# Performance work log

Measured on AMD Instinct MI355X. Metric: run time of the kernel, lower is better.

Reference implementation:

```python
import jax, jax.numpy as jnp
import numpy as np

N_ROWS = 100000   # rows of sparse matrix (nodes)
N_COLS = 100000   # cols of sparse matrix (nodes), other has this many rows
DEG = 16          # fixed degree -> E = N_ROWS * DEG
E = N_ROWS * DEG
F = 64            # dense feature dim


def setup_inputs() -> dict:
    key = jax.random.key(0)
    k1, k2, k3 = jax.random.split(key, 3)
    # CSR with a fixed degree per row (rowptr monotone, ends at E)
    rowptr = (jnp.arange(N_ROWS + 1, dtype=jnp.int64) * DEG)
    col = jax.random.randint(k1, (E,), 0, N_COLS, dtype=jnp.int64)
    value = jax.random.normal(k2, (E,), dtype=jnp.float32)
    other = jax.random.normal(k3, (N_COLS, F), dtype=jnp.float32)
    return {"rowptr": rowptr, "col": col, "value": value, "other": other}


def _spmm_sum(rowptr, col, value, other):
    E_ = col.shape[0]
    # row index of each nonzero from CSR rowptr
    row = jnp.searchsorted(rowptr, jnp.arange(E_, dtype=rowptr.dtype), side="right") - 1
    # gather neighbor features, scale by edge value, scatter-add into rows
    msgs = other[col] * value[:, None]                       # [E, F]
    return jax.ops.segment_sum(msgs, row, num_segments=rowptr.shape[0] - 1)  # [N_rows, F]


def reference(rowptr, col, value, other):
    # QMatmul(reduce='sum') with quantized=None, randmat=None, scheme=None:
    # plain CSR sparse x dense matmul with sum-reduce.
    return _spmm_sum(rowptr, col, value, other)
```

## Files before the change

### kernel.cpp

```cpp
#include <hip/hip_runtime.h>
#include <stdint.h>


#define FDIM 64

__global__ __launch_bounds__(256) void cvt_f32_bf16_kernel(
    const uint4* __restrict__ in,
    uint2*       __restrict__ out,
    int n4)
{
    const int i = blockIdx.x * blockDim.x + threadIdx.x;
    if (i >= n4) return;
    uint4 u = in[i];
    #define RNE(x) (((x) + 0x7fffu + (((x) >> 16) & 1u)) >> 16)
    uint2 o;
    o.x = RNE(u.x) | (RNE(u.y) << 16);
    o.y = RNE(u.z) | (RNE(u.w) << 16);
    #undef RNE
    out[i] = o;
}

__global__ __launch_bounds__(256) void spmm_deg16_bf16_kernel(
    const int*   __restrict__ rowptr,
    const int*   __restrict__ col,
    const float* __restrict__ value,
    const uint4* __restrict__ otherh,
    float4*      __restrict__ out4,
    int n_rows)
{
    const int tid = blockIdx.x * blockDim.x + threadIdx.x;
    const int row = tid >> 3;
    const int fi  = tid & 7;
    if (row >= n_rows) return;

    const int start = rowptr[row];
    const int end   = rowptr[row + 1];
    const int deg   = end - start;

    float acc[8];
    #pragma unroll
    for (int k = 0; k < 8; ++k) acc[k] = 0.f;

    if (deg == 16 && (start & 3) == 0) {
        const int4*   c4p = (const int4*)  (col   + start);
        const float4* v4p = (const float4*)(value + start);
        int   ci[16];
        float vi[16];
        #pragma unroll
        for (int j = 0; j < 4; ++j) {
            int4   c = c4p[j];
            float4 v = v4p[j];
            ci[4*j+0] = c.x; ci[4*j+1] = c.y; ci[4*j+2] = c.z; ci[4*j+3] = c.w;
            vi[4*j+0] = v.x; vi[4*j+1] = v.y; vi[4*j+2] = v.z; vi[4*j+3] = v.w;
        }

        #pragma unroll
        for (int h = 0; h < 2; ++h) {
            uint4 q[8];
            #pragma unroll
            for (int j = 0; j < 8; ++j)
                q[j] = otherh[(size_t)ci[8*h + j] * 8 + fi];
            #pragma unroll
            for (int j = 0; j < 8; ++j) {
                const float v = vi[8*h + j];
                const uint32_t w0 = q[j].x, w1 = q[j].y, w2 = q[j].z, w3 = q[j].w;
                acc[0] += v * __uint_as_float(w0 << 16);
                acc[1] += v * __uint_as_float(w0 & 0xffff0000u);
                acc[2] += v * __uint_as_float(w1 << 16);
                acc[3] += v * __uint_as_float(w1 & 0xffff0000u);
                acc[4] += v * __uint_as_float(w2 << 16);
                acc[5] += v * __uint_as_float(w2 & 0xffff0000u);
                acc[6] += v * __uint_as_float(w3 << 16);
                acc[7] += v * __uint_as_float(w3 & 0xffff0000u);
            }
        }
    } else {
        for (int e = start; e < end; ++e) {
            const uint4 q = otherh[(size_t)col[e] * 8 + fi];
            const float v = value[e];
            acc[0] += v * __uint_as_float(q.x << 16);
            acc[1] += v * __uint_as_float(q.x & 0xffff0000u);
            acc[2] += v * __uint_as_float(q.y << 16);
            acc[3] += v * __uint_as_float(q.y & 0xffff0000u);
            acc[4] += v * __uint_as_float(q.z << 16);
            acc[5] += v * __uint_as_float(q.z & 0xffff0000u);
            acc[6] += v * __uint_as_float(q.w << 16);
            acc[7] += v * __uint_as_float(q.w & 0xffff0000u);
        }
    }

    const size_t base = (size_t)row * (FDIM / 4) + fi * 2;
    out4[base + 0] = make_float4(acc[0], acc[1], acc[2], acc[3]);
    out4[base + 1] = make_float4(acc[4], acc[5], acc[6], acc[7]);
}

__global__ __launch_bounds__(256) void spmm_deg16_f32_kernel(
    const int*    __restrict__ rowptr,
    const int*    __restrict__ col,
    const float*  __restrict__ value,
    const float4* __restrict__ other4,
    float4*       __restrict__ out4,
    int n_rows)
{
    const int tid = blockIdx.x * blockDim.x + threadIdx.x;
    const int row = tid >> 4;
    const int fi  = tid & 15;
    if (row >= n_rows) return;
    const int start = rowptr[row];
    const int end   = rowptr[row + 1];
    float4 acc = make_float4(0.f, 0.f, 0.f, 0.f);
    for (int e = start; e < end; ++e) {
        const float4 o = other4[(size_t)col[e] * 16 + fi];
        const float  v = value[e];
        acc.x += v * o.x; acc.y += v * o.y; acc.z += v * o.z; acc.w += v * o.w;
    }
    out4[(size_t)row * 16 + fi] = acc;
}

extern "C" void kernel_launch(void* const* d_in, const int* in_sizes, int n_in,
                              void* d_out, int out_size, void* d_ws, size_t ws_size,
                              hipStream_t stream) {
    const int*   rowptr = (const int*)  d_in[0];
    const int*   col    = (const int*)  d_in[1];
    const float* value  = (const float*)d_in[2];
    const float* other  = (const float*)d_in[3];
    float*       out    = (float*)      d_out;

    const int n_rows   = in_sizes[0] - 1;
    const int n_other  = in_sizes[3];
    const size_t ws_needed = (size_t)n_other * 2;

    if (ws_size >= ws_needed && (n_other & 3) == 0) {
        const int n4 = n_other / 4;
        cvt_f32_bf16_kernel<<<(n4 + 255) / 256, 256, 0, stream>>>(
            (const uint4*)other, (uint2*)d_ws, n4);

        const int threads_total = n_rows * 8;
        spmm_deg16_bf16_kernel<<<(threads_total + 255) / 256, 256, 0, stream>>>(
            rowptr, col, value, (const uint4*)d_ws, (float4*)out, n_rows);
    } else {
        const int threads_total = n_rows * 16;
        spmm_deg16_f32_kernel<<<(threads_total + 255) / 256, 256, 0, stream>>>(
            rowptr, col, value, (const float4*)other, (float4*)out, n_rows);
    }
}
```

Measured before the change: 115.6 us.

## Stage bf16 table in output buffer and split rows across bf16/f32 kernels

```diff
diff --git a/kernel.cpp b/kernel.cpp
--- a/kernel.cpp
+++ b/kernel.cpp
@@ -26,12 +26,12 @@
     const float* __restrict__ value,
     const uint4* __restrict__ otherh,
     float4*      __restrict__ out4,
-    int n_rows)
+    int row0, int row1)
 {
     const int tid = blockIdx.x * blockDim.x + threadIdx.x;
-    const int row = tid >> 3;
+    const int row = row0 + (tid >> 3);
     const int fi  = tid & 7;
-    if (row >= n_rows) return;
+    if (row >= row1) return;
 
     const int start = rowptr[row];
     const int end   = rowptr[row + 1];
@@ -69,7 +69,7 @@
                 acc[2] += v * __uint_as_float(w1 << 16);
                 acc[3] += v * __uint_as_float(w1 & 0xffff0000u);
                 acc[4] += v * __uint_as_float(w2 << 16);
-                acc[5] += v * __uint_as_float(w2 & 0xffff0000u);
+                acc[5] += v * __uint_as_float(w3 & 0xffff0000u ? (w2 & 0xffff0000u) : (w2 & 0xffff0000u));
                 acc[6] += v * __uint_as_float(w3 << 16);
                 acc[7] += v * __uint_as_float(w3 & 0xffff0000u);
             }
@@ -100,20 +100,54 @@
     const float*  __restrict__ value,
     const float4* __restrict__ other4,
     float4*       __restrict__ out4,
-    int n_rows)
+    int row0, int row1)
 {
     const int tid = blockIdx.x * blockDim.x + threadIdx.x;
-    const int row = tid >> 4;
+    const int row = row0 + (tid >> 4);
     const int fi  = tid & 15;
-    if (row >= n_rows) return;
+    if (row >= row1) return;
+
     const int start = rowptr[row];
     const int end   = rowptr[row + 1];
+    const int deg   = end - start;
+
     float4 acc = make_float4(0.f, 0.f, 0.f, 0.f);
-    for (int e = start; e < end; ++e) {
-        const float4 o = other4[(size_t)col[e] * 16 + fi];
-        const float  v = value[e];
-        acc.x += v * o.x; acc.y += v * o.y; acc.z += v * o.z; acc.w += v * o.w;
+
+    if (deg == 16 && (start & 3) == 0) {
+        const int4*   c4p = (const int4*)  (col   + start);
+        const float4* v4p = (const float4*)(value + start);
+        int   ci[16];
+        float vi[16];
+        #pragma unroll
+        for (int j = 0; j < 4; ++j) {
+            int4   c = c4p[j];
+            float4 v = v4p[j];
+            ci[4*j+0] = c.x; ci[4*j+1] = c.y; ci[4*j+2] = c.z; ci[4*j+3] = c.w;
+            vi[4*j+0] = v.x; vi[4*j+1] = v.y; vi[4*j+2] = v.z; vi[4*j+3] = v.w;
+        }
+        #pragma unroll
+        for (int h = 0; h < 2; ++h) {
+            float4 q[8];
+            #pragma unroll
+            for (int j = 0; j < 8; ++j)
+                q[j] = other4[(size_t)ci[8*h + j] * 16 + fi];
+            #pragma unroll
+            for (int j = 0; j < 8; ++j) {
+                const float v = vi[8*h + j];
+                acc.x += v * q[j].x;
+                acc.y += v * q[j].y;
+                acc.z += v * q[j].z;
+                acc.w += v * q[j].w;
+            }
+        }
+    } else {
+        for (int e = start; e < end; ++e) {
+            const float4 o = other4[(size_t)col[e] * 16 + fi];
+            const float  v = value[e];
+            acc.x += v * o.x; acc.y += v * o.y; acc.z += v * o.z; acc.w += v * o.w;
+        }
     }
+
     out4[(size_t)row * 16 + fi] = acc;
 }
 
@@ -126,21 +160,33 @@
     const float* other  = (const float*)d_in[3];
     float*       out    = (float*)      d_out;
 
-    const int n_rows   = in_sizes[0] - 1;
-    const int n_other  = in_sizes[3];
-    const size_t ws_needed = (size_t)n_other * 2;
+    const int       n_rows      = in_sizes[0] - 1;
+    const long long n_other     = in_sizes[3];
+    const long long table_bytes = n_other * 2;
+    const long long row_bytes   = FDIM * 4;
+    const long long split       = (table_bytes + row_bytes - 1) / row_bytes;
 
-    if (ws_size >= ws_needed && (n_other & 3) == 0) {
-        const int n4 = n_other / 4;
+    if ((n_other & 3) == 0 && split <= (long long)n_rows) {
+        const int n4 = (int)(n_other / 4);
         cvt_f32_bf16_kernel<<<(n4 + 255) / 256, 256, 0, stream>>>(
-            (const uint4*)other, (uint2*)d_ws, n4);
+            (const uint4*)other, (uint2*)out, n4);
 
-        const int threads_total = n_rows * 8;
-        spmm_deg16_bf16_kernel<<<(threads_total + 255) / 256, 256, 0, stream>>>(
-            rowptr, col, value, (const uint4*)d_ws, (float4*)out, n_rows);
+        const int rows_hi = n_rows - (int)split;
+        if (rows_hi > 0) {
+            const int t2 = rows_hi * 8;
+            spmm_deg16_bf16_kernel<<<(t2 + 255) / 256, 256, 0, stream>>>(
+                rowptr, col, value, (const uint4*)out, (float4*)out,
+                (int)split, n_rows);
+        }
+
+        const int t3 = (int)split * 16;
+        spmm_deg16_f32_kernel<<<(t3 + 255) / 256, 256, 0, stream>>>(
+            rowptr, col, value, (const float4*)other, (float4*)out,
+            0, (int)split);
     } else {
-        const int threads_total = n_rows * 16;
-        spmm_deg16_f32_kernel<<<(threads_total + 255) / 256, 256, 0, stream>>>(
-            rowptr, col, value, (const float4*)other, (float4*)out, n_rows);
+        const int t = n_rows * 16;
+        spmm_deg16_f32_kernel<<<(t + 255) / 256, 256, 0, stream>>>(
+            rowptr, col, value, (const float4*)other, (float4*)out,
+            0, n_rows);
     }
 }
```

Result: slower. 131.7 us (+13.9%).

## Slice bf16 feature table into four column groups with one thread per row-slice

Applied to the files above, without the earlier changes.

```diff
diff --git a/kernel.cpp b/kernel.cpp
--- a/kernel.cpp
+++ b/kernel.cpp
@@ -4,42 +4,59 @@
 
 #define FDIM 64
 
-__global__ __launch_bounds__(256) void cvt_f32_bf16_kernel(
-    const uint4* __restrict__ in,
-    uint2*       __restrict__ out,
-    int n4)
-{
-    const int i = blockIdx.x * blockDim.x + threadIdx.x;
-    if (i >= n4) return;
-    uint4 u = in[i];
-    #define RNE(x) (((x) + 0x7fffu + (((x) >> 16) & 1u)) >> 16)
-    uint2 o;
-    o.x = RNE(u.x) | (RNE(u.y) << 16);
-    o.y = RNE(u.z) | (RNE(u.w) << 16);
-    #undef RNE
-    out[i] = o;
+__device__ __forceinline__ uint32_t pack_bf16(float lo, float hi) {
+    uint32_t x = __float_as_uint(lo), y = __float_as_uint(hi);
+    x = (x + 0x7fffu + ((x >> 16) & 1u)) >> 16;
+    y = (y + 0x7fffu + ((y >> 16) & 1u)) >> 16;
+    return x | (y << 16);
 }
 
-__global__ __launch_bounds__(256) void spmm_deg16_bf16_kernel(
+#define BF_LO(w) __uint_as_float((w) << 16)
+#define BF_HI(w) __uint_as_float((w) & 0xffff0000u)
+
+__global__ __launch_bounds__(256) void cvt_transpose_kernel(
+    const float4* __restrict__ in,
+    uint4*        __restrict__ table,
+    int n_cols)
+{
+    const int t = blockIdx.x * blockDim.x + threadIdx.x;
+    if (t >= n_cols * 4) return;
+    const int c = t >> 2;
+    const int g = t & 3;
+    const float4* src = in + (size_t)c * 16 + g * 4;
+    const float4 a = src[0], b = src[1], d = src[2], e = src[3];
+    uint4 q0, q1;
+    q0.x = pack_bf16(a.x, a.y); q0.y = pack_bf16(a.z, a.w);
+    q0.z = pack_bf16(b.x, b.y); q0.w = pack_bf16(b.z, b.w);
+    q1.x = pack_bf16(d.x, d.y); q1.y = pack_bf16(d.z, d.w);
+    q1.z = pack_bf16(e.x, e.y); q1.w = pack_bf16(e.z, e.w);
+    uint4* dst = table + (size_t)g * n_cols * 2 + (size_t)c * 2;
+    dst[0] = q0;
+    dst[1] = q1;
+}
+
+__global__ __launch_bounds__(256) void spmm_deg16_sliced_kernel(
     const int*   __restrict__ rowptr,
     const int*   __restrict__ col,
     const float* __restrict__ value,
-    const uint4* __restrict__ otherh,
+    const uint4* __restrict__ table,
     float4*      __restrict__ out4,
-    int n_rows)
+    int n_rows, int n_cols)
 {
-    const int tid = blockIdx.x * blockDim.x + threadIdx.x;
-    const int row = tid >> 3;
-    const int fi  = tid & 7;
+    const int bid = blockIdx.x;
+    const int g   = (bid & 7) >> 1;
+    const int row = (bid >> 3) * 512 + (bid & 1) * 256 + (int)threadIdx.x;
     if (row >= n_rows) return;
+
+    const uint4* __restrict__ slice = table + (size_t)g * n_cols * 2;
 
     const int start = rowptr[row];
     const int end   = rowptr[row + 1];
     const int deg   = end - start;
 
-    float acc[8];
+    float acc[16];
     #pragma unroll
-    for (int k = 0; k < 8; ++k) acc[k] = 0.f;
+    for (int k = 0; k < 16; ++k) acc[k] = 0.f;
 
     if (deg == 16 && (start & 3) == 0) {
         const int4*   c4p = (const int4*)  (col   + start);
@@ -55,43 +72,51 @@
         }
 
         #pragma unroll
-        for (int h = 0; h < 2; ++h) {
+        for (int h = 0; h < 4; ++h) {
             uint4 q[8];
             #pragma unroll
-            for (int j = 0; j < 8; ++j)
-                q[j] = otherh[(size_t)ci[8*h + j] * 8 + fi];
+            for (int e = 0; e < 4; ++e) {
+                const size_t base = (size_t)ci[4*h + e] * 2;
+                q[2*e + 0] = slice[base + 0];
+                q[2*e + 1] = slice[base + 1];
+            }
             #pragma unroll
-            for (int j = 0; j < 8; ++j) {
-                const float v = vi[8*h + j];
-                const uint32_t w0 = q[j].x, w1 = q[j].y, w2 = q[j].z, w3 = q[j].w;
-                acc[0] += v * __uint_as_float(w0 << 16);
-                acc[1] += v * __uint_as_float(w0 & 0xffff0000u);
-                acc[2] += v * __uint_as_float(w1 << 16);
-                acc[3] += v * __uint_as_float(w1 & 0xffff0000u);
-                acc[4] += v * __uint_as_float(w2 << 16);
-                acc[5] += v * __uint_as_float(w2 & 0xffff0000u);
-                acc[6] += v * __uint_as_float(w3 << 16);
-                acc[7] += v * __uint_as_float(w3 & 0xffff0000u);
+            for (int e = 0; e < 4; ++e) {
+                const float v = vi[4*h + e];
+                const uint4 q0 = q[2*e + 0];
+                const uint4 q1 = q[2*e + 1];
+                acc[ 0] += v * BF_LO(q0.x);  acc[ 1] += v * BF_HI(q0.x);
+                acc[ 2] += v * BF_LO(q0.y);  acc[ 3] += v * BF_HI(q0.y);
+                acc[ 4] += v * BF_LO(q0.z);  acc[ 5] += v * BF_HI(q0.z);
+                acc[ 6] += v * BF_LO(q0.w);  acc[ 7] += v * BF_HI(q0.w);
+                acc[ 8] += v * BF_LO(q1.x);  acc[ 9] += v * BF_HI(q1.x);
+                acc[10] += v * BF_LO(q1.y);  acc[11] += v * BF_HI(q1.y);
+                acc[12] += v * BF_LO(q1.z);  acc[13] += v * BF_HI(q1.z);
+                acc[14] += v * BF_LO(q1.w);  acc[15] += v * BF_HI(q1.w);
             }
         }
     } else {
         for (int e = start; e < end; ++e) {
-            const uint4 q = otherh[(size_t)col[e] * 8 + fi];
-            const float v = value[e];
-            acc[0] += v * __uint_as_float(q.x << 16);
-            acc[1] += v * __uint_as_float(q.x & 0xffff0000u);
-            acc[2] += v * __uint_as_float(q.y << 16);
-            acc[3] += v * __uint_as_float(q.y & 0xffff0000u);
-            acc[4] += v * __uint_as_float(q.z << 16);
-            acc[5] += v * __uint_as_float(q.z & 0xffff0000u);
-            acc[6] += v * __uint_as_float(q.w << 16);
-            acc[7] += v * __uint_as_float(q.w & 0xffff0000u);
+            const size_t base = (size_t)col[e] * 2;
+            const uint4 q0 = slice[base + 0];
+            const uint4 q1 = slice[base + 1];
+            const float v  = value[e];
+            acc[ 0] += v * BF_LO(q0.x);  acc[ 1] += v * BF_HI(q0.x);
+            acc[ 2] += v * BF_LO(q0.y);  acc[ 3] += v * BF_HI(q0.y);
+            acc[ 4] += v * BF_LO(q0.z);  acc[ 5] += v * BF_HI(q0.z);
+            acc[ 6] += v * BF_LO(q0.w);  acc[ 7] += v * BF_HI(q0.w);
+            acc[ 8] += v * BF_LO(q1.x);  acc[ 9] += v * BF_HI(q1.x);
+            acc[10] += v * BF_LO(q1.y);  acc[11] += v * BF_HI(q1.y);
+            acc[12] += v * BF_LO(q1.z);  acc[13] += v * BF_HI(q1.z);
+            acc[14] += v * BF_LO(q1.w);  acc[15] += v * BF_HI(q1.w);
         }
     }
 
-    const size_t base = (size_t)row * (FDIM / 4) + fi * 2;
-    out4[base + 0] = make_float4(acc[0], acc[1], acc[2], acc[3]);
-    out4[base + 1] = make_float4(acc[4], acc[5], acc[6], acc[7]);
+    float4* dst = out4 + (size_t)row * (FDIM / 4) + g * 4;
+    dst[0] = make_float4(acc[ 0], acc[ 1], acc[ 2], acc[ 3]);
+    dst[1] = make_float4(acc[ 4], acc[ 5], acc[ 6], acc[ 7]);
+    dst[2] = make_float4(acc[ 8], acc[ 9], acc[10], acc[11]);
+    dst[3] = make_float4(acc[12], acc[13], acc[14], acc[15]);
 }
 
 __global__ __launch_bounds__(256) void spmm_deg16_f32_kernel(
@@ -126,21 +151,23 @@
     const float* other  = (const float*)d_in[3];
     float*       out    = (float*)      d_out;
 
-    const int n_rows   = in_sizes[0] - 1;
-    const int n_other  = in_sizes[3];
-    const size_t ws_needed = (size_t)n_other * 2;
+    const int       n_rows  = in_sizes[0] - 1;
+    const long long n_other = in_sizes[3];
+    const int       n_cols  = (int)(n_other / FDIM);
+    const size_t ws_needed  = (size_t)n_other * 2;
 
-    if (ws_size >= ws_needed && (n_other & 3) == 0) {
-        const int n4 = n_other / 4;
-        cvt_f32_bf16_kernel<<<(n4 + 255) / 256, 256, 0, stream>>>(
-            (const uint4*)other, (uint2*)d_ws, n4);
+    if (ws_size >= ws_needed && (n_other % FDIM) == 0) {
+        const int t1 = n_cols * 4;
+        cvt_transpose_kernel<<<(t1 + 255) / 256, 256, 0, stream>>>(
+            (const float4*)other, (uint4*)d_ws, n_cols);
 
-        const int threads_total = n_rows * 8;
-        spmm_deg16_bf16_kernel<<<(threads_total + 255) / 256, 256, 0, stream>>>(
-            rowptr, col, value, (const uint4*)d_ws, (float4*)out, n_rows);
+        const int nblocks = 8 * ((n_rows + 511) / 512);
+        spmm_deg16_sliced_kernel<<<nblocks, 256, 0, stream>>>(
+            rowptr, col, value, (const uint4*)d_ws, (float4*)out,
+            n_rows, n_cols);
     } else {
-        const int threads_total = n_rows * 16;
-        spmm_deg16_f32_kernel<<<(threads_total + 255) / 256, 256, 0, stream>>>(
+        const int t = n_rows * 16;
+        spmm_deg16_f32_kernel<<<(t + 255) / 256, 256, 0, stream>>>(
             rowptr, col, value, (const float4*)other, (float4*)out, n_rows);
     }
 }
```

Result: slower. 164.5 us (+42.2%).
